# Performance work log

Hardware: AMD Instinct MI355X
Metric: run time of the kernel (lower is better)

## Reference

```python
import jax, jax.numpy as jnp
import numpy as np

HIDDEN = 1024
INTER = 4096
N_EXPERTS = 8


def geglu(x, w1, w2, w3):
    # x: [N, C], w1/w2: [C, I], w3: [I, C]
    return (jax.nn.gelu(x @ w1, approximate=False) * (x @ w2)) @ w3


def setup_inputs() -> dict:
    key = jax.random.key(0)
    ks = jax.random.split(key, 8)
    s = 0.02
    x = jax.random.normal(ks[0], (2, 2048, HIDDEN), dtype=jnp.float32)
    w1s = jax.random.normal(ks[1], (HIDDEN, INTER), dtype=jnp.float32) * s
    w2s = jax.random.normal(ks[2], (HIDDEN, INTER), dtype=jnp.float32) * s
    w3s = jax.random.normal(ks[3], (INTER, HIDDEN), dtype=jnp.float32) * s
    W1 = jax.random.normal(ks[4], (N_EXPERTS, HIDDEN, INTER), dtype=jnp.float32) * s
    W2 = jax.random.normal(ks[5], (N_EXPERTS, HIDDEN, INTER), dtype=jnp.float32) * s
    W3 = jax.random.normal(ks[6], (N_EXPERTS, INTER, HIDDEN), dtype=jnp.float32) * s
    Wg = jax.random.normal(ks[7], (HIDDEN, N_EXPERTS), dtype=jnp.float32) * s
    return {"x": x, "w1s": w1s, "w2s": w2s, "w3s": w3s,
            "W1": W1, "W2": W2, "W3": W3, "Wg": Wg}


def reference(x, w1s, w2s, w3s, W1, W2, W3, Wg):
    B, T, C = x.shape
    xf = x.reshape(-1, C)  # [N, C]
    shared = geglu(xf, w1s, w2s, w3s)  # [N, C]
    logits = xf @ Wg  # [N, E]
    # top-1 of softmax == argmax of logits (softmax is monotone);
    # NOTE: original torch code does NOT multiply by the routing prob.
    idx = jnp.argmax(logits, axis=-1)  # [N]
    final = jnp.zeros_like(xf)
    for e in range(N_EXPERTS):  # small fixed expert count
        y = geglu(xf, W1[e], W2[e], W3[e])  # [N, C]
        final = final + jnp.where((idx == e)[:, None], y, 0.0)
    return (shared + final).reshape(B, T, C)
```

## Files before the change

### kernel.cpp

```cpp
#include <hip/hip_runtime.h>
#include <stdint.h>

#define HIDDEN 1024
#define INTER  4096
#define NTOK   4096
#define HROWS  (2*NTOK)
#define BK     64
#define MAXB1  40
#define MAXB2  72
#define NMAT   27
#define TPM    512

typedef unsigned short u16;
typedef unsigned int   u32;
typedef __bf16  bf16x8 __attribute__((ext_vector_type(8)));
typedef float   f32x4  __attribute__((ext_vector_type(4)));
typedef u32     u32x4  __attribute__((ext_vector_type(4)));

__device__ __forceinline__ u16 f2bf(float f) {
  u32 u = __float_as_uint(f);
  u32 r = u + 0x7FFFu + ((u >> 16) & 1u);
  return (u16)(r >> 16);
}

__device__ __forceinline__ u32 cvt_pk_bf16(float lo, float hi) {
  u32 r;
  asm("v_cvt_pk_bf16_f32 %0, %1, %2" : "=v"(r) : "v"(lo), "v"(hi));
  return r;
}

__device__ __forceinline__ void glds16(const void* g, void* l) {
  __builtin_amdgcn_global_load_lds(
      (const __attribute__((address_space(1))) void*)g,
      (__attribute__((address_space(3))) void*)l, 16, 0, 0);
}


__global__ void k_init(int* cnt, int* fill) {
  if (threadIdx.x < 8) { cnt[threadIdx.x] = 0; fill[threadIdx.x] = 0; }
}

__global__ __launch_bounds__(256) void k_gate(const float* __restrict__ x,
                                              const float* __restrict__ wg,
                                              int* __restrict__ idx,
                                              int* __restrict__ cnt) {
  int wave = threadIdx.x >> 6, lane = threadIdx.x & 63;
  int t = blockIdx.x * 4 + wave;
  if (t >= NTOK) return;
  float acc[8];
  #pragma unroll
  for (int e = 0; e < 8; ++e) acc[e] = 0.f;
  const float* xr = x + (size_t)t * HIDDEN;
  for (int c = lane; c < HIDDEN; c += 64) {
    float xv = xr[c];
    const float* wrow = wg + (size_t)c * 8;
    #pragma unroll
    for (int e = 0; e < 8; ++e) acc[e] += xv * wrow[e];
  }
  #pragma unroll
  for (int e = 0; e < 8; ++e)
    for (int s = 32; s; s >>= 1) acc[e] += __shfl_xor(acc[e], s);
  if (lane == 0) {
    int best = 0; float bv = acc[0];
    #pragma unroll
    for (int e = 1; e < 8; ++e) if (acc[e] > bv) { bv = acc[e]; best = e; }
    idx[t] = best;
    atomicAdd(&cnt[best], 1);
  }
}

__global__ void k_cvt(const float* __restrict__ x, u16* __restrict__ xb, int n4) {
  int i = blockIdx.x * blockDim.x + threadIdx.x;
  if (i >= n4) return;
  float4 v = ((const float4*)x)[i];
  ushort4 o;
  o.x = f2bf(v.x); o.y = f2bf(v.y); o.z = f2bf(v.z); o.w = f2bf(v.w);
  ((ushort4*)xb)[i] = o;
}

__global__ void k_table(const int* __restrict__ cnt, int* __restrict__ off,
                        int4* __restrict__ tab1, int* __restrict__ nblk1,
                        int4* __restrict__ tab2, int* __restrict__ nblk2) {
  if (threadIdx.x != 0 || blockIdx.x != 0) return;
  int o = 0;
  int offs[8];
  for (int e = 0; e < 8; ++e) { offs[e] = o; off[e] = o; o += cnt[e]; }
  int nb = 0;
  for (int m = 0; m < NTOK / 256; ++m)
    tab1[nb++] = make_int4(8, m * 256, 256, 0);
  for (int e = 0; e < 8; ++e)
    for (int j = 0; j * 256 < cnt[e]; ++j) {
      int rows = cnt[e] - j * 256; if (rows > 256) rows = 256;
      tab1[nb++] = make_int4(e, NTOK + offs[e] + j * 256, rows, offs[e] + j * 256);
    }
  *nblk1 = nb;
  nb = 0;
  for (int m = 0; m < NTOK / 128; ++m)
    tab2[nb++] = make_int4(8, m * 128, 128, 0);
  for (int e = 0; e < 8; ++e)
    for (int j = 0; j * 128 < cnt[e]; ++j) {
      int rows = cnt[e] - j * 128; if (rows > 128) rows = 128;
      tab2[nb++] = make_int4(e, NTOK + offs[e] + j * 128, rows, offs[e] + j * 128);
    }
  *nblk2 = nb;
}

__global__ void k_scatter(const int* __restrict__ idx, const int* __restrict__ off,
                          int* __restrict__ fill, int* __restrict__ perm) {
  int t = blockIdx.x * blockDim.x + threadIdx.x;
  if (t >= NTOK) return;
  int e = idx[t];
  int p = atomicAdd(&fill[e], 1);
  perm[off[e] + p] = t;
}


__global__ __launch_bounds__(256) void k_wcvt(
    const float* __restrict__ w1s, const float* __restrict__ w2s,
    const float* __restrict__ w3s, const float* __restrict__ W1,
    const float* __restrict__ W2,  const float* __restrict__ W3,
    u16* __restrict__ Wb)
{
  int bid = blockIdx.x;
  int m = bid >> 9;
  int tile = bid & (TPM - 1);
  const float* src; int N, kt, pp;
  if (m < 18) {
    N = INTER;
    int mm = (m < 9) ? m : m - 9;
    const float* sp = (m < 9) ? w1s : w2s;
    const float* ep = (m < 9) ? W1 : W2;
    src = (mm == 0) ? sp : ep + (size_t)(mm - 1) * HIDDEN * INTER;
    kt = tile >> 5; pp = tile & 31;
  } else {
    N = HIDDEN;
    int mm = m - 18;
    src = (mm == 0) ? w3s : W3 + (size_t)(mm - 1) * INTER * HIDDEN;
    kt = tile >> 3; pp = tile & 7;
  }

  __shared__ float tileF[64 * 128];
  int tid = threadIdx.x;
  const float* in0 = src + (size_t)(kt * 64) * N + pp * 128;
  #pragma unroll
  for (int i = 0; i < 8; ++i) {
    int f = tid + 256 * i;
    int k = f >> 5, c4 = f & 31;
    *(float4*)&tileF[k * 128 + c4 * 4] = *(const float4*)(in0 + (size_t)k * N + c4 * 4);
  }
  __syncthreads();

  int n = tid >> 1;
  int ph = (tid & 1) * 4;
  u16* outp = Wb + (size_t)bid * 8192 + n * 64 + ph * 8;
  #pragma unroll
  for (int j = 0; j < 4; ++j) {
    int p8 = ph + j;
    int k8 = p8 ^ (n & 7);
    const float* col = &tileF[(k8 * 8) * 128 + n];
    u32x4 pk;
    pk.x = cvt_pk_bf16(col[0],   col[128]);
    pk.y = cvt_pk_bf16(col[256], col[384]);
    pk.z = cvt_pk_bf16(col[512], col[640]);
    pk.w = cvt_pk_bf16(col[768], col[896]);
    *(u32x4*)(outp + j * 8) = pk;
  }
}


__global__ __launch_bounds__(512, 2) void k_mlp1(
    const u16* __restrict__ xb, const u16* __restrict__ Wb,
    const int* __restrict__ perm, const int4* __restrict__ tab,
    const int* __restrict__ nblk, u16* __restrict__ Hbuf)
{
  int bx = blockIdx.x;
  if (bx >= *nblk) return;
  int4 te = tab[bx];
  int g = te.x, hrow0 = te.y, rows = te.z, pb = te.w;
  int m1 = (g == 8) ? 0 : 1 + g;
  int pp = blockIdx.y;
  int nbase = pp * 128;

  extern __shared__ __align__(16) char smem[];
  int tid = threadIdx.x;
  int w = tid >> 6, lane = tid & 63;
  int q = lane >> 4, rl = lane & 15;
  int mw = w >> 2, nw = w & 3;

  int tokj[4];
  #pragma unroll
  for (int j = 0; j < 4; ++j) {
    int r = w * 32 + j * 8 + (lane >> 3);
    int rc = (r < rows) ? r : (rows - 1);
    tokj[j] = (g == 8) ? (hrow0 + rc) : perm[pb + rc];
  }
  int schunk = (lane & 7) ^ ((lane >> 3) & 7);

  const char* pB1 = (const char*)(Wb + ((size_t)m1 * TPM + pp) * 8192);
  const char* pB2 = (const char*)(Wb + ((size_t)(m1 + 9) * TPM + pp) * 8192);

  f32x4 acc1[8][2], acc2[8][2];
  f32x4 z = {0.f, 0.f, 0.f, 0.f};
  #pragma unroll
  for (int mi = 0; mi < 8; ++mi)
    #pragma unroll
    for (int ni = 0; ni < 2; ++ni) { acc1[mi][ni] = z; acc2[mi][ni] = z; }

  auto STAGE = [&](char* L, int kt) {
    int k0 = kt * BK;
    #pragma unroll
    for (int j = 0; j < 4; ++j) {
      const char* src = (const char*)xb + ((size_t)tokj[j] * HIDDEN + k0) * 2 + schunk * 16;
      glds16(src, L + w * 4096 + j * 1024);
    }
    size_t ko = (size_t)kt * 32 * 16384;
    #pragma unroll
    for (int j = 0; j < 2; ++j) {
      int o = w * 2048 + j * 1024;
      glds16(pB1 + ko + o + lane * 16, L + 32768 + o);
      glds16(pB2 + ko + o + lane * 16, L + 49152 + o);
    }
  };

  auto COMPUTE = [&](const char* Lc) {
    const u16* LA  = (const u16*)Lc;
    const u16* LB1 = (const u16*)(Lc + 32768);
    const u16* LB2 = (const u16*)(Lc + 49152);
    #pragma unroll
    for (int ks = 0; ks < 2; ++ks) {
      int co = (((ks << 2) | q) ^ (rl & 7)) * 8;
      bf16x8 af[8], b1[2], b2[2];
      #pragma unroll
      for (int mi = 0; mi < 8; ++mi)
        af[mi] = *(const bf16x8*)&LA[(mw * 128 + mi * 16 + rl) * 64 + co];
      #pragma unroll
      for (int ni = 0; ni < 2; ++ni) {
        int n = nw * 32 + ni * 16 + rl;
        b1[ni] = *(const bf16x8*)&LB1[n * 64 + co];
        b2[ni] = *(const bf16x8*)&LB2[n * 64 + co];
      }
      #pragma unroll
      for (int mi = 0; mi < 8; ++mi)
        #pragma unroll
        for (int ni = 0; ni < 2; ++ni) {
          acc1[mi][ni] = __builtin_amdgcn_mfma_f32_16x16x32_bf16(af[mi], b1[ni], acc1[mi][ni], 0, 0, 0);
          acc2[mi][ni] = __builtin_amdgcn_mfma_f32_16x16x32_bf16(af[mi], b2[ni], acc2[mi][ni], 0, 0, 0);
        }
    }
  };

  char* L0 = smem;
  char* L1 = smem + 65536;
  STAGE(L0, 0);
  asm volatile("s_waitcnt vmcnt(0)" ::: "memory");
  __syncthreads();
  int cur = 0;
  for (int kt = 0; kt < HIDDEN / BK; ++kt) {
    char* Lc = cur ? L1 : L0;
    char* Ln = cur ? L0 : L1;
    if (kt < HIDDEN / BK - 1) STAGE(Ln, kt + 1);
    COMPUTE(Lc);
    if (kt < HIDDEN / BK - 1) {
      asm volatile("s_waitcnt vmcnt(0)" ::: "memory");
      __syncthreads();
      cur ^= 1;
    }
  }

  #pragma unroll
  for (int mi = 0; mi < 8; ++mi) {
    #pragma unroll
    for (int j = 0; j < 4; ++j) {
      int r = mw * 128 + mi * 16 + q * 4 + j;
      if (r < rows) {
        size_t hb = (size_t)(hrow0 + r) * INTER + nbase + nw * 32;
        #pragma unroll
        for (int ni = 0; ni < 2; ++ni) {
          float h1 = acc1[mi][ni][j];
          float h2 = acc2[mi][ni][j];
          float ge = 0.5f * h1 * (1.0f + erff(h1 * 0.7071067811865476f));
          Hbuf[hb + ni * 16 + rl] = f2bf(ge * h2);
        }
      }
    }
  }
}


__global__ __launch_bounds__(256, 2) void k_mlp2(
    const u16* __restrict__ Hbuf, const u16* __restrict__ Wb,
    const int* __restrict__ perm, const int4* __restrict__ tab,
    const int* __restrict__ nblk, float* __restrict__ out,
    float* __restrict__ yexp)
{
  int bx = blockIdx.x;
  if (bx >= *nblk) return;
  int4 te = tab[bx];
  int g = te.x, hrow0 = te.y, rows = te.z, pb = te.w;
  int m3 = (g == 8) ? 18 : 19 + g;
  int pp = blockIdx.y;
  int nbase = pp * 128;

  extern __shared__ __align__(16) char smem[];
  int tid = threadIdx.x;
  int w = tid >> 6, lane = tid & 63;
  int q = lane >> 4, rl = lane & 15;
  int wr = (w >> 1) * 64, wc = (w & 1) * 64;

  int hr[4];
  #pragma unroll
  for (int j = 0; j < 4; ++j) {
    int r = w * 32 + j * 8 + (lane >> 3);
    int rc = (r < rows) ? r : (rows - 1);
    hr[j] = hrow0 + rc;
  }
  int schunk = (lane & 7) ^ ((lane >> 3) & 7);

  const char* pB = (const char*)(Wb + ((size_t)m3 * TPM + pp) * 8192);

  f32x4 acc[4][4];
  f32x4 z = {0.f, 0.f, 0.f, 0.f};
  #pragma unroll
  for (int mi = 0; mi < 4; ++mi)
    #pragma unroll
    for (int ni = 0; ni < 4; ++ni) acc[mi][ni] = z;

  auto STAGE = [&](char* L, int kt) {
    int k0 = kt * BK;
    #pragma unroll
    for (int j = 0; j < 4; ++j) {
      const char* src = (const char*)Hbuf + ((size_t)hr[j] * INTER + k0) * 2 + schunk * 16;
      glds16(src, L + w * 4096 + j * 1024);
    }
    size_t ko = (size_t)kt * 8 * 16384;
    #pragma unroll
    for (int j = 0; j < 4; ++j) {
      int o = w * 4096 + j * 1024;
      glds16(pB + ko + o + lane * 16, L + 16384 + o);
    }
  };

  auto COMPUTE = [&](const char* Lc) {
    const u16* LA = (const u16*)Lc;
    const u16* LB = (const u16*)(Lc + 16384);
    #pragma unroll
    for (int ks = 0; ks < 2; ++ks) {
      int co = (((ks << 2) | q) ^ (rl & 7)) * 8;
      bf16x8 af[4], bf[4];
      #pragma unroll
      for (int mi = 0; mi < 4; ++mi)
        af[mi] = *(const bf16x8*)&LA[(wr + mi * 16 + rl) * 64 + co];
      #pragma unroll
      for (int ni = 0; ni < 4; ++ni)
        bf[ni] = *(const bf16x8*)&LB[(wc + ni * 16 + rl) * 64 + co];
      #pragma unroll
      for (int mi = 0; mi < 4; ++mi)
        #pragma unroll
        for (int ni = 0; ni < 4; ++ni)
          acc[mi][ni] = __builtin_amdgcn_mfma_f32_16x16x32_bf16(af[mi], bf[ni], acc[mi][ni], 0, 0, 0);
    }
  };

  char* L0 = smem;
  char* L1 = smem + 32768;
  STAGE(L0, 0);
  asm volatile("s_waitcnt vmcnt(0)" ::: "memory");
  __syncthreads();
  int cur = 0;
  for (int kt = 0; kt < INTER / BK; ++kt) {
    char* Lc = cur ? L1 : L0;
    char* Ln = cur ? L0 : L1;
    if (kt < INTER / BK - 1) STAGE(Ln, kt + 1);
    COMPUTE(Lc);
    if (kt < INTER / BK - 1) {
      asm volatile("s_waitcnt vmcnt(0)" ::: "memory");
      __syncthreads();
      cur ^= 1;
    }
  }

  float* dstb = (g == 8) ? out : yexp;
  #pragma unroll
  for (int mi = 0; mi < 4; ++mi) {
    #pragma unroll
    for (int j = 0; j < 4; ++j) {
      int r = wr + mi * 16 + q * 4 + j;
      if (r < rows) {
        int tok = (g == 8) ? (hrow0 + r) : perm[pb + r];
        size_t ob = (size_t)tok * HIDDEN + nbase + wc;
        #pragma unroll
        for (int ni = 0; ni < 4; ++ni)
          dstb[ob + ni * 16 + rl] = acc[mi][ni][j];
      }
    }
  }
}

__global__ void k_add(float* __restrict__ out, const float* __restrict__ yexp, int n4) {
  int i = blockIdx.x * blockDim.x + threadIdx.x;
  if (i >= n4) return;
  float4 a = ((const float4*)out)[i];
  float4 b = ((const float4*)yexp)[i];
  a.x += b.x; a.y += b.y; a.z += b.z; a.w += b.w;
  ((float4*)out)[i] = a;
}


extern "C" void kernel_launch(void* const* d_in, const int* in_sizes, int n_in,
                              void* d_out, int out_size, void* d_ws, size_t ws_size,
                              hipStream_t stream) {
  const float* x   = (const float*)d_in[0];
  const float* w1s = (const float*)d_in[1];
  const float* w2s = (const float*)d_in[2];
  const float* w3s = (const float*)d_in[3];
  const float* W1  = (const float*)d_in[4];
  const float* W2  = (const float*)d_in[5];
  const float* W3  = (const float*)d_in[6];
  const float* Wg  = (const float*)d_in[7];
  float* out = (float*)d_out;

  char* ws = (char*)d_ws;
  size_t o_xb   = 0;
  size_t o_H    = o_xb   + (size_t)NTOK * HIDDEN * 2;
  size_t o_yexp = o_H    + (size_t)HROWS * INTER * 2;
  size_t o_Wb   = o_yexp + (size_t)NTOK * HIDDEN * 4;
  size_t o_idx  = o_Wb   + (size_t)NMAT * TPM * 16384;
  size_t o_perm = o_idx  + (size_t)NTOK * 4;
  size_t o_cnt  = o_perm + (size_t)NTOK * 4;
  size_t o_off  = o_cnt  + 32;
  size_t o_fill = o_off  + 32;
  size_t o_nb1  = o_fill + 32;
  size_t o_nb2  = o_nb1  + 32;
  size_t o_tab1 = o_nb2  + 32;
  size_t o_tab2 = o_tab1 + (size_t)MAXB1 * 16;
  size_t need   = o_tab2 + (size_t)MAXB2 * 16;
  if (ws_size < need) return;

  u16*  xb   = (u16*)(ws + o_xb);
  u16*  Hbuf = (u16*)(ws + o_H);
  float* yexp = (float*)(ws + o_yexp);
  u16*  Wb   = (u16*)(ws + o_Wb);
  int*  idx  = (int*)(ws + o_idx);
  int*  perm = (int*)(ws + o_perm);
  int*  cnt  = (int*)(ws + o_cnt);
  int*  off  = (int*)(ws + o_off);
  int*  fill = (int*)(ws + o_fill);
  int*  nblk1 = (int*)(ws + o_nb1);
  int*  nblk2 = (int*)(ws + o_nb2);
  int4* tab1 = (int4*)(ws + o_tab1);
  int4* tab2 = (int4*)(ws + o_tab2);

  k_init<<<1, 64, 0, stream>>>(cnt, fill);
  k_gate<<<NTOK / 4, 256, 0, stream>>>(x, Wg, idx, cnt);
  k_cvt<<<(NTOK * HIDDEN / 4) / 256, 256, 0, stream>>>(x, xb, NTOK * HIDDEN / 4);
  k_wcvt<<<NMAT * TPM, 256, 0, stream>>>(w1s, w2s, w3s, W1, W2, W3, Wb);
  k_table<<<1, 1, 0, stream>>>(cnt, off, tab1, nblk1, tab2, nblk2);
  k_scatter<<<NTOK / 256, 256, 0, stream>>>(idx, off, fill, perm);
  k_mlp1<<<dim3(MAXB1, INTER / 128), 512, 131072, stream>>>(xb, Wb, perm, tab1, nblk1, Hbuf);
  k_mlp2<<<dim3(MAXB2, HIDDEN / 128), 256, 65536, stream>>>(Hbuf, Wb, perm, tab2, nblk2, out, yexp);
  k_add<<<(NTOK * HIDDEN / 4) / 256, 256, 0, stream>>>(out, yexp, NTOK * HIDDEN / 4);
}
```

Before: 539.8 us.

## Switch GEMMs to BK=32 four-stage LDS pipeline with partial vmcnt waits

Both MoE GEMM kernels move from a double-buffered BK=64 loop with a full vmcnt(0) drain each step to a four-slot BK=32 ring that stays three stages ahead. Each step waits only on the oldest loads via counted vmcnt waits, and MFMA sections run at raised wave priority. The weight pre-conversion layout changes to 32-wide K tiles to match, and mlp2 grows to 512 threads with 256-column output tiles. The aim is to hide global-load latency behind compute, at the cost of more barriers per K and lower arithmetic per stage.

```diff
diff --git a/kernel.cpp b/kernel.cpp
--- a/kernel.cpp
+++ b/kernel.cpp
@@ -5,17 +5,23 @@
 #define INTER  4096
 #define NTOK   4096
 #define HROWS  (2*NTOK)
-#define BK     64
 #define MAXB1  40
 #define MAXB2  72
 #define NMAT   27
-#define TPM    512
 
 typedef unsigned short u16;
 typedef unsigned int   u32;
 typedef __bf16  bf16x8 __attribute__((ext_vector_type(8)));
 typedef float   f32x4  __attribute__((ext_vector_type(4)));
 typedef u32     u32x4  __attribute__((ext_vector_type(4)));
+
+#define WAITVM(N) asm volatile("s_waitcnt vmcnt(" #N ")" ::: "memory")
+
+__device__ __forceinline__ void hard_barrier() {
+  asm volatile("" ::: "memory");
+  __builtin_amdgcn_s_barrier();
+  asm volatile("" ::: "memory");
+}
 
 __device__ __forceinline__ u16 f2bf(float f) {
   u32 u = __float_as_uint(f);
@@ -122,48 +128,45 @@
     u16* __restrict__ Wb)
 {
   int bid = blockIdx.x;
-  int m = bid >> 9;
-  int tile = bid & (TPM - 1);
-  const float* src; int N, kt, pp;
+  int m = bid >> 9, pair = bid & 511;
+  const float* src; int N, Tp, kt, pp2;
   if (m < 18) {
-    N = INTER;
+    N = INTER; Tp = 32;
     int mm = (m < 9) ? m : m - 9;
     const float* sp = (m < 9) ? w1s : w2s;
     const float* ep = (m < 9) ? W1 : W2;
     src = (mm == 0) ? sp : ep + (size_t)(mm - 1) * HIDDEN * INTER;
-    kt = tile >> 5; pp = tile & 31;
+    kt = pair >> 4; pp2 = pair & 15;
   } else {
-    N = HIDDEN;
+    N = HIDDEN; Tp = 8;
     int mm = m - 18;
     src = (mm == 0) ? w3s : W3 + (size_t)(mm - 1) * INTER * HIDDEN;
-    kt = tile >> 3; pp = tile & 7;
-  }
-
-  __shared__ float tileF[64 * 128];
+    kt = pair >> 2; pp2 = pair & 3;
+  }
+
+  __shared__ float tileF[32 * 256];
   int tid = threadIdx.x;
-  const float* in0 = src + (size_t)(kt * 64) * N + pp * 128;
+  const float* in0 = src + (size_t)(kt * 32) * N + pp2 * 256;
   #pragma unroll
   for (int i = 0; i < 8; ++i) {
     int f = tid + 256 * i;
-    int k = f >> 5, c4 = f & 31;
-    *(float4*)&tileF[k * 128 + c4 * 4] = *(const float4*)(in0 + (size_t)k * N + c4 * 4);
+    int k = f >> 6, c4 = f & 63;
+    *(float4*)&tileF[k * 256 + c4 * 4] = *(const float4*)(in0 + (size_t)k * N + c4 * 4);
   }
   __syncthreads();
 
-  int n = tid >> 1;
-  int ph = (tid & 1) * 4;
-  u16* outp = Wb + (size_t)bid * 8192 + n * 64 + ph * 8;
-  #pragma unroll
-  for (int j = 0; j < 4; ++j) {
-    int p8 = ph + j;
-    int k8 = p8 ^ (n & 7);
-    const float* col = &tileF[(k8 * 8) * 128 + n];
+  int p2 = tid >> 7, n = tid & 127;
+  u16* outp = Wb + ((size_t)m * 1024 + kt * Tp + pp2 * 2 + p2) * 4096 + n * 32;
+  #pragma unroll
+  for (int s = 0; s < 4; ++s) {
+    int k8 = s ^ ((n >> 1) & 3);
+    const float* col = &tileF[(k8 * 8) * 256 + p2 * 128 + n];
     u32x4 pk;
-    pk.x = cvt_pk_bf16(col[0],   col[128]);
-    pk.y = cvt_pk_bf16(col[256], col[384]);
-    pk.z = cvt_pk_bf16(col[512], col[640]);
-    pk.w = cvt_pk_bf16(col[768], col[896]);
-    *(u32x4*)(outp + j * 8) = pk;
+    pk.x = cvt_pk_bf16(col[0],    col[256]);
+    pk.y = cvt_pk_bf16(col[512],  col[768]);
+    pk.z = cvt_pk_bf16(col[1024], col[1280]);
+    pk.w = cvt_pk_bf16(col[1536], col[1792]);
+    *(u32x4*)(outp + s * 8) = pk;
   }
 }
 
@@ -187,17 +190,17 @@
   int q = lane >> 4, rl = lane & 15;
   int mw = w >> 2, nw = w & 3;
 
-  int tokj[4];
-  #pragma unroll
-  for (int j = 0; j < 4; ++j) {
-    int r = w * 32 + j * 8 + (lane >> 3);
+  int tokj[2];
+  #pragma unroll
+  for (int j = 0; j < 2; ++j) {
+    int r = w * 32 + j * 16 + (lane >> 2);
     int rc = (r < rows) ? r : (rows - 1);
     tokj[j] = (g == 8) ? (hrow0 + rc) : perm[pb + rc];
   }
-  int schunk = (lane & 7) ^ ((lane >> 3) & 7);
-
-  const char* pB1 = (const char*)(Wb + ((size_t)m1 * TPM + pp) * 8192);
-  const char* pB2 = (const char*)(Wb + ((size_t)(m1 + 9) * TPM + pp) * 8192);
+  int gch = ((lane & 3) ^ ((lane >> 3) & 3)) * 16;
+
+  const char* pB1 = (const char*)Wb + ((size_t)m1 * 1024 + pp) * 8192;
+  const char* pB2 = (const char*)Wb + ((size_t)(m1 + 9) * 1024 + pp) * 8192;
 
   f32x4 acc1[8][2], acc2[8][2];
   f32x4 z = {0.f, 0.f, 0.f, 0.f};
@@ -206,65 +209,57 @@
     #pragma unroll
     for (int ni = 0; ni < 2; ++ni) { acc1[mi][ni] = z; acc2[mi][ni] = z; }
 
-  auto STAGE = [&](char* L, int kt) {
-    int k0 = kt * BK;
-    #pragma unroll
-    for (int j = 0; j < 4; ++j) {
-      const char* src = (const char*)xb + ((size_t)tokj[j] * HIDDEN + k0) * 2 + schunk * 16;
-      glds16(src, L + w * 4096 + j * 1024);
-    }
-    size_t ko = (size_t)kt * 32 * 16384;
+  auto STAGE = [&](int t) {
+    char* L = smem + (t & 3) * 32768;
+    int k0 = t * 32;
     #pragma unroll
     for (int j = 0; j < 2; ++j) {
-      int o = w * 2048 + j * 1024;
-      glds16(pB1 + ko + o + lane * 16, L + 32768 + o);
-      glds16(pB2 + ko + o + lane * 16, L + 49152 + o);
-    }
+      const char* src = (const char*)xb + ((size_t)tokj[j] * HIDDEN + k0) * 2 + gch;
+      glds16(src, L + w * 2048 + j * 1024);
+    }
+    glds16(pB1 + (size_t)t * 262144 + (tid << 4), L + 16384 + w * 1024);
+    glds16(pB2 + (size_t)t * 262144 + (tid << 4), L + 24576 + w * 1024);
   };
 
-  auto COMPUTE = [&](const char* Lc) {
-    const u16* LA  = (const u16*)Lc;
-    const u16* LB1 = (const u16*)(Lc + 32768);
-    const u16* LB2 = (const u16*)(Lc + 49152);
-    #pragma unroll
-    for (int ks = 0; ks < 2; ++ks) {
-      int co = (((ks << 2) | q) ^ (rl & 7)) * 8;
-      bf16x8 af[8], b1[2], b2[2];
-      #pragma unroll
-      for (int mi = 0; mi < 8; ++mi)
-        af[mi] = *(const bf16x8*)&LA[(mw * 128 + mi * 16 + rl) * 64 + co];
+  int co = (q ^ ((rl >> 1) & 3)) * 8;
+
+  auto COMPUTE = [&](int t) {
+    const u16* LA  = (const u16*)(smem + (t & 3) * 32768);
+    const u16* LB1 = LA + 8192;
+    const u16* LB2 = LA + 12288;
+    bf16x8 af[8], b1[2], b2[2];
+    #pragma unroll
+    for (int mi = 0; mi < 8; ++mi)
+      af[mi] = *(const bf16x8*)&LA[(mw * 128 + mi * 16 + rl) * 32 + co];
+    #pragma unroll
+    for (int ni = 0; ni < 2; ++ni) {
+      int n = nw * 32 + ni * 16 + rl;
+      b1[ni] = *(const bf16x8*)&LB1[n * 32 + co];
+      b2[ni] = *(const bf16x8*)&LB2[n * 32 + co];
+    }
+    __builtin_amdgcn_s_setprio(1);
+    #pragma unroll
+    for (int mi = 0; mi < 8; ++mi)
       #pragma unroll
       for (int ni = 0; ni < 2; ++ni) {
-        int n = nw * 32 + ni * 16 + rl;
-        b1[ni] = *(const bf16x8*)&LB1[n * 64 + co];
-        b2[ni] = *(const bf16x8*)&LB2[n * 64 + co];
+        acc1[mi][ni] = __builtin_amdgcn_mfma_f32_16x16x32_bf16(af[mi], b1[ni], acc1[mi][ni], 0, 0, 0);
+        acc2[mi][ni] = __builtin_amdgcn_mfma_f32_16x16x32_bf16(af[mi], b2[ni], acc2[mi][ni], 0, 0, 0);
       }
-      #pragma unroll
-      for (int mi = 0; mi < 8; ++mi)
-        #pragma unroll
-        for (int ni = 0; ni < 2; ++ni) {
-          acc1[mi][ni] = __builtin_amdgcn_mfma_f32_16x16x32_bf16(af[mi], b1[ni], acc1[mi][ni], 0, 0, 0);
-          acc2[mi][ni] = __builtin_amdgcn_mfma_f32_16x16x32_bf16(af[mi], b2[ni], acc2[mi][ni], 0, 0, 0);
-        }
-    }
+    __builtin_amdgcn_s_setprio(0);
   };
 
-  char* L0 = smem;
-  char* L1 = smem + 65536;
-  STAGE(L0, 0);
-  asm volatile("s_waitcnt vmcnt(0)" ::: "memory");
-  __syncthreads();
-  int cur = 0;
-  for (int kt = 0; kt < HIDDEN / BK; ++kt) {
-    char* Lc = cur ? L1 : L0;
-    char* Ln = cur ? L0 : L1;
-    if (kt < HIDDEN / BK - 1) STAGE(Ln, kt + 1);
-    COMPUTE(Lc);
-    if (kt < HIDDEN / BK - 1) {
-      asm volatile("s_waitcnt vmcnt(0)" ::: "memory");
-      __syncthreads();
-      cur ^= 1;
-    }
+  const int NT = HIDDEN / 32;
+  STAGE(0); STAGE(1); STAGE(2);
+  for (int t = 0; t < NT; ++t) {
+    if (t + 3 < NT) STAGE(t + 3);
+    int rem = NT - 1 - t;
+    if (rem >= 3)      WAITVM(12);
+    else if (rem == 2) WAITVM(8);
+    else if (rem == 1) WAITVM(4);
+    else               WAITVM(0);
+    hard_barrier();
+    COMPUTE(t);
+    hard_barrier();
   }
 
   #pragma unroll
@@ -287,7 +282,7 @@
 }
 
 
-__global__ __launch_bounds__(256, 2) void k_mlp2(
+__global__ __launch_bounds__(512, 2) void k_mlp2(
     const u16* __restrict__ Hbuf, const u16* __restrict__ Wb,
     const int* __restrict__ perm, const int4* __restrict__ tab,
     const int* __restrict__ nblk, float* __restrict__ out,
@@ -298,25 +293,20 @@
   int4 te = tab[bx];
   int g = te.x, hrow0 = te.y, rows = te.z, pb = te.w;
   int m3 = (g == 8) ? 18 : 19 + g;
-  int pp = blockIdx.y;
-  int nbase = pp * 128;
+  int pp2 = blockIdx.y;
 
   extern __shared__ __align__(16) char smem[];
   int tid = threadIdx.x;
   int w = tid >> 6, lane = tid & 63;
   int q = lane >> 4, rl = lane & 15;
-  int wr = (w >> 1) * 64, wc = (w & 1) * 64;
-
-  int hr[4];
-  #pragma unroll
-  for (int j = 0; j < 4; ++j) {
-    int r = w * 32 + j * 8 + (lane >> 3);
-    int rc = (r < rows) ? r : (rows - 1);
-    hr[j] = hrow0 + rc;
-  }
-  int schunk = (lane & 7) ^ ((lane >> 3) & 7);
-
-  const char* pB = (const char*)(Wb + ((size_t)m3 * TPM + pp) * 8192);
+  int mw = w >> 2, nw = w & 3;
+
+  int rr = w * 16 + (lane >> 2);
+  int rc = (rr < rows) ? rr : (rows - 1);
+  int hr = hrow0 + rc;
+  int gch = ((lane & 3) ^ ((lane >> 3) & 3)) * 16;
+
+  const char* pB = (const char*)Wb + ((size_t)m3 * 1024 + pp2 * 2) * 8192;
 
   f32x4 acc[4][4];
   f32x4 z = {0.f, 0.f, 0.f, 0.f};
@@ -325,58 +315,51 @@
     #pragma unroll
     for (int ni = 0; ni < 4; ++ni) acc[mi][ni] = z;
 
-  auto STAGE = [&](char* L, int kt) {
-    int k0 = kt * BK;
-    #pragma unroll
-    for (int j = 0; j < 4; ++j) {
-      const char* src = (const char*)Hbuf + ((size_t)hr[j] * INTER + k0) * 2 + schunk * 16;
-      glds16(src, L + w * 4096 + j * 1024);
-    }
-    size_t ko = (size_t)kt * 8 * 16384;
-    #pragma unroll
-    for (int j = 0; j < 4; ++j) {
-      int o = w * 4096 + j * 1024;
-      glds16(pB + ko + o + lane * 16, L + 16384 + o);
-    }
+  auto STAGE = [&](int t) {
+    char* L = smem + (t & 3) * 24576;
+    int k0 = t * 32;
+    const char* src = (const char*)Hbuf + ((size_t)hr * INTER + k0) * 2 + gch;
+    glds16(src, L + w * 1024);
+    #pragma unroll
+    for (int j = 0; j < 2; ++j)
+      glds16(pB + (size_t)t * 65536 + j * 8192 + (tid << 4), L + 8192 + j * 8192 + w * 1024);
   };
 
-  auto COMPUTE = [&](const char* Lc) {
-    const u16* LA = (const u16*)Lc;
-    const u16* LB = (const u16*)(Lc + 16384);
-    #pragma unroll
-    for (int ks = 0; ks < 2; ++ks) {
-      int co = (((ks << 2) | q) ^ (rl & 7)) * 8;
-      bf16x8 af[4], bf[4];
-      #pragma unroll
-      for (int mi = 0; mi < 4; ++mi)
-        af[mi] = *(const bf16x8*)&LA[(wr + mi * 16 + rl) * 64 + co];
+  int co = (q ^ ((rl >> 1) & 3)) * 8;
+
+  auto COMPUTE = [&](int t) {
+    const u16* LA = (const u16*)(smem + (t & 3) * 24576);
+    const u16* LB = LA + 4096;
+    bf16x8 af[4], bf[4];
+    #pragma unroll
+    for (int mi = 0; mi < 4; ++mi)
+      af[mi] = *(const bf16x8*)&LA[(mw * 64 + mi * 16 + rl) * 32 + co];
+    #pragma unroll
+    for (int ni = 0; ni < 4; ++ni) {
+      int n = nw * 64 + ni * 16 + rl;
+      bf[ni] = *(const bf16x8*)&LB[n * 32 + co];
+    }
+    __builtin_amdgcn_s_setprio(1);
+    #pragma unroll
+    for (int mi = 0; mi < 4; ++mi)
       #pragma unroll
       for (int ni = 0; ni < 4; ++ni)
-        bf[ni] = *(const bf16x8*)&LB[(wc + ni * 16 + rl) * 64 + co];
-      #pragma unroll
-      for (int mi = 0; mi < 4; ++mi)
-        #pragma unroll
-        for (int ni = 0; ni < 4; ++ni)
-          acc[mi][ni] = __builtin_amdgcn_mfma_f32_16x16x32_bf16(af[mi], bf[ni], acc[mi][ni], 0, 0, 0);
-    }
+        acc[mi][ni] = __builtin_amdgcn_mfma_f32_16x16x32_bf16(af[mi], bf[ni], acc[mi][ni], 0, 0, 0);
+    __builtin_amdgcn_s_setprio(0);
   };
 
-  char* L0 = smem;
-  char* L1 = smem + 32768;
-  STAGE(L0, 0);
-  asm volatile("s_waitcnt vmcnt(0)" ::: "memory");
-  __syncthreads();
-  int cur = 0;
-  for (int kt = 0; kt < INTER / BK; ++kt) {
-    char* Lc = cur ? L1 : L0;
-    char* Ln = cur ? L0 : L1;
-    if (kt < INTER / BK - 1) STAGE(Ln, kt + 1);
-    COMPUTE(Lc);
-    if (kt < INTER / BK - 1) {
-      asm volatile("s_waitcnt vmcnt(0)" ::: "memory");
-      __syncthreads();
-      cur ^= 1;
-    }
+  const int NT = INTER / 32;
+  STAGE(0); STAGE(1); STAGE(2);
+  for (int t = 0; t < NT; ++t) {
+    if (t + 3 < NT) STAGE(t + 3);
+    int rem = NT - 1 - t;
+    if (rem >= 3)      WAITVM(9);
+    else if (rem == 2) WAITVM(6);
+    else if (rem == 1) WAITVM(3);
+    else               WAITVM(0);
+    hard_barrier();
+    COMPUTE(t);
+    hard_barrier();
   }
 
   float* dstb = (g == 8) ? out : yexp;
@@ -384,10 +367,10 @@
   for (int mi = 0; mi < 4; ++mi) {
     #pragma unroll
     for (int j = 0; j < 4; ++j) {
-      int r = wr + mi * 16 + q * 4 + j;
+      int r = mw * 64 + mi * 16 + q * 4 + j;
       if (r < rows) {
         int tok = (g == 8) ? (hrow0 + r) : perm[pb + r];
-        size_t ob = (size_t)tok * HIDDEN + nbase + wc;
+        size_t ob = (size_t)tok * HIDDEN + pp2 * 256 + nw * 64;
         #pragma unroll
         for (int ni = 0; ni < 4; ++ni)
           dstb[ob + ni * 16 + rl] = acc[mi][ni][j];
@@ -424,7 +407,7 @@
   size_t o_H    = o_xb   + (size_t)NTOK * HIDDEN * 2;
   size_t o_yexp = o_H    + (size_t)HROWS * INTER * 2;
   size_t o_Wb   = o_yexp + (size_t)NTOK * HIDDEN * 4;
-  size_t o_idx  = o_Wb   + (size_t)NMAT * TPM * 16384;
+  size_t o_idx  = o_Wb   + (size_t)NMAT * 1024 * 8192;
   size_t o_perm = o_idx  + (size_t)NTOK * 4;
   size_t o_cnt  = o_perm + (size_t)NTOK * 4;
   size_t o_off  = o_cnt  + 32;
@@ -453,10 +436,10 @@
   k_init<<<1, 64, 0, stream>>>(cnt, fill);
   k_gate<<<NTOK / 4, 256, 0, stream>>>(x, Wg, idx, cnt);
   k_cvt<<<(NTOK * HIDDEN / 4) / 256, 256, 0, stream>>>(x, xb, NTOK * HIDDEN / 4);
-  k_wcvt<<<NMAT * TPM, 256, 0, stream>>>(w1s, w2s, w3s, W1, W2, W3, Wb);
+  k_wcvt<<<NMAT * 512, 256, 0, stream>>>(w1s, w2s, w3s, W1, W2, W3, Wb);
   k_table<<<1, 1, 0, stream>>>(cnt, off, tab1, nblk1, tab2, nblk2);
   k_scatter<<<NTOK / 256, 256, 0, stream>>>(idx, off, fill, perm);
   k_mlp1<<<dim3(MAXB1, INTER / 128), 512, 131072, stream>>>(xb, Wb, perm, tab1, nblk1, Hbuf);
-  k_mlp2<<<dim3(MAXB2, HIDDEN / 128), 256, 65536, stream>>>(Hbuf, Wb, perm, tab2, nblk2, out, yexp);
+  k_mlp2<<<dim3(MAXB2, HIDDEN / 256), 512, 98304, stream>>>(Hbuf, Wb, perm, tab2, nblk2, out, yexp);
   k_add<<<(NTOK * HIDDEN / 4) / 256, 256, 0, stream>>>(out, yexp, NTOK * HIDDEN / 4);
 }
```

Result: slower. 561.7 us (+4.1%).
